# Performance work log

Hardware: AMD Instinct MI355X
Metric: run time of the kernel (lower is better)

The kernel has to match this reference:

```python
import jax, jax.numpy as jnp
import numpy as np


def setup_inputs() -> dict:
    key = jax.random.key(0)
    kx, kb, ky = jax.random.split(key, 3)
    N, K, D = 100000, 256, 3
    x = jax.random.normal(kx, (N, D), dtype=jnp.float32)
    # beta in (0, 1) for atanh; cap below 1 to keep atanh finite
    beta = jax.random.uniform(kb, (N,), dtype=jnp.float32, minval=0.01, maxval=0.95)
    # y in {-1, 0..K-1}; -1 = background. Guarantee both classes present.
    y = jax.random.randint(ky, (N,), -1, K)
    y = y.at[0].set(-1).at[1].set(0)
    return {"x": x, "beta": beta, "y": y, "K": K, "S_b": 1.0, "q_min": 0.5}


def reference(x, beta, y, K, S_b, q_min):
    N = y.shape[0]
    n_i = (y == -1)  # background mask (N,)
    # One-hot membership M_ik (N, K); jax.nn.one_hot gives all-zeros for y == -1
    M = jax.nn.one_hot(y, K, dtype=x.dtype)

    # ---- background loss ----
    beta_ak = jnp.max(beta[:, None] * M, axis=0)               # (K,) segment max
    N_b = jnp.sum(n_i).astype(x.dtype)
    L_beta = jnp.sum(1.0 - beta_ak) / K \
        + (S_b / N_b) * jnp.sum(jnp.where(n_i, beta, 0.0))

    # ---- potential loss ----
    q_i = jnp.square(jnp.arctanh(beta)) + q_min               # (N,) charge
    qM = q_i[:, None] * M                                      # (N, K)
    q_ak = jnp.max(qM, axis=0)                                 # (K,) max charge per cluster
    idx_ak = jnp.argmax(qM, axis=0)                            # (K,) condensation point index
    x_a = x[idx_ak]                                            # (K, D) cluster rep coords
    # pairwise squared distances hit->cluster rep: (N, K)
    x_diff = jnp.sum(jnp.square(x[:, None, :] - x_a[None, :, :]), axis=2)
    x_inv = jnp.maximum(1.0 - x_diff, 0.0)                     # repulsive potential
    # attractive for members, repulsive for non-members, weighted by q_ak and q_i
    per_hit = jnp.sum((M * x_diff + (1.0 - M) * x_inv) * q_ak[None, :], axis=1)
    L_v = jnp.sum(per_hit * q_i) / N

    return L_beta + L_v
```

## Files before the change

### kernel.cpp

```cpp
#include <hip/hip_runtime.h>
#include <math.h>

#define K_MAX 256
#define P1 64
#define NT 256

struct Ws {
    unsigned long long part_packed[P1 * K_MAX];
    unsigned int       part_beta[P1 * K_MAX];
    float              part_bg[P1];
    float              part_nb[P1];
    float4             cvec[K_MAX];
    float              qv[K_MAX];
    float              bak[K_MAX];
    float              bg_total;
    float              nb_total;
};

__device__ __forceinline__ float wave_sum(float v) {
    #pragma unroll
    for (int o = 32; o > 0; o >>= 1) v += __shfl_down(v, o, 64);
    return v;
}

__global__ void __launch_bounds__(NT) k_scan(const float* __restrict__ beta,
        const int* __restrict__ y, const float* __restrict__ qminp,
        Ws* __restrict__ w, int N) {
    __shared__ unsigned long long s_u64[K_MAX];
    __shared__ unsigned int s_u32[K_MAX];
    __shared__ float s_w[8];
    int t = threadIdx.x;
    int b = blockIdx.x;
    s_u64[t] = 0ULL;
    s_u32[t] = 0u;
    __syncthreads();
    float qmin = qminp[0];
    float bg = 0.f, nbc = 0.f;
    for (int i = b * NT + t; i < N; i += P1 * NT) {
        float be = beta[i];
        int yi = y[i];
        if (yi < 0) { bg += be; nbc += 1.f; }
        else {
            atomicMax(&s_u32[yi], __float_as_uint(be));
            float a = atanhf(be);
            float q = fmaf(a, a, qmin);
            unsigned long long p = ((unsigned long long)__float_as_uint(q) << 32)
                                 | (unsigned long long)(~(unsigned int)i);
            atomicMax(&s_u64[yi], p);
        }
    }
    __syncthreads();
    w->part_packed[b * K_MAX + t] = s_u64[t];
    w->part_beta[b * K_MAX + t]  = s_u32[t];
    int lane = t & 63, wid = t >> 6;
    float r1 = wave_sum(bg);
    float r2 = wave_sum(nbc);
    if (lane == 0) { s_w[wid] = r1; s_w[4 + wid] = r2; }
    __syncthreads();
    if (t == 0) w->part_bg[b] = s_w[0] + s_w[1] + s_w[2] + s_w[3];
    if (t == 1) w->part_nb[b] = s_w[4] + s_w[5] + s_w[6] + s_w[7];
}

__global__ void __launch_bounds__(64) k_reduce(const float* __restrict__ x,
        Ws* __restrict__ w, float* __restrict__ out) {
    int b = blockIdx.x, t = threadIdx.x;
    if (b < K_MAX) {
        unsigned long long m = w->part_packed[t * K_MAX + b];
        unsigned int bb = w->part_beta[t * K_MAX + b];
        #pragma unroll
        for (int o = 32; o > 0; o >>= 1) {
            unsigned long long v = __shfl_down(m, o, 64);  if (v > m)  m = v;
            unsigned int       u = __shfl_down(bb, o, 64); if (u > bb) bb = u;
        }
        if (t == 0) {
            float q; unsigned int idx;
            if (m == 0ULL) { q = 0.f; idx = 0u; }
            else { q = __uint_as_float((unsigned int)(m >> 32)); idx = ~(unsigned int)m; }
            float ax = x[idx * 3], ay = x[idx * 3 + 1], az = x[idx * 3 + 2];
            w->cvec[b] = make_float4(2.f * q * ax, 2.f * q * ay, 2.f * q * az,
                                     q * (1.f - (ax * ax + ay * ay + az * az)));
            w->qv[b]  = q;
            w->bak[b] = 1.f - __uint_as_float(bb);
        }
    } else {
        const float* src = (b == K_MAX) ? w->part_bg : w->part_nb;
        float s = wave_sum(src[t]);
        if (t == 0) {
            if (b == K_MAX) { w->bg_total = s; out[0] = 0.f; }
            else            { w->nb_total = s; }
        }
    }
}

__global__ void __launch_bounds__(NT) k_main(const float* __restrict__ x,
        const float* __restrict__ beta, const int* __restrict__ y,
        const int* __restrict__ Kp, const float* __restrict__ Sbp,
        const float* __restrict__ qminp, const Ws* __restrict__ w,
        float* __restrict__ out, int N) {
    __shared__ float4 s_c[K_MAX];
    __shared__ float s_q[K_MAX];
    __shared__ float s_w[8];
    int t = threadIdx.x;
    s_c[t] = w->cvec[t];
    s_q[t] = w->qv[t];
    __syncthreads();
    int i = blockIdx.x * NT + t;
    float contrib = 0.f;
    if (i < N) {
        float x0 = x[i * 3], x1 = x[i * 3 + 1], x2 = x[i * 3 + 2];
        float be = beta[i];
        int yi = y[i];
        float a = atanhf(be);
        float qi = fmaf(a, a, qminp[0]);
        float negh = -(x0 * x0 + x1 * x1 + x2 * x2);
        float acc = 0.f;
        #pragma unroll 8
        for (int k = 0; k < K_MAX; ++k) {
            float4 c = s_c[k];
            float t0 = fmaf(s_q[k], negh, c.w);
            float uq = fmaf(c.x, x0, fmaf(c.y, x1, fmaf(c.z, x2, t0)));
            acc += fmaxf(uq, 0.f);
        }
        if (yi >= 0) {
            float4 c = s_c[yi];
            float qk = s_q[yi];
            float t0 = fmaf(qk, negh, c.w);
            float uq = fmaf(c.x, x0, fmaf(c.y, x1, fmaf(c.z, x2, t0)));
            acc += (qk - uq) - fmaxf(uq, 0.f);
        }
        contrib = acc * qi;
    }
    int lane = t & 63, wid = t >> 6;
    float r = wave_sum(contrib);
    if (lane == 0) s_w[wid] = r;
    __syncthreads();
    if (t == 0) atomicAdd(out, (s_w[0] + s_w[1] + s_w[2] + s_w[3]) * (1.f / (float)N));
    if (blockIdx.x == 0) {
        int K = Kp[0];
        float v = wave_sum((t < K) ? w->bak[t] : 0.f);
        if (lane == 0) s_w[4 + wid] = v;
        __syncthreads();
        if (t == 0) {
            float sb = s_w[4] + s_w[5] + s_w[6] + s_w[7];
            atomicAdd(out, sb / (float)K + Sbp[0] / w->nb_total * w->bg_total);
        }
    }
}

extern "C" void kernel_launch(void* const* d_in, const int* in_sizes, int n_in,
                              void* d_out, int out_size, void* d_ws, size_t ws_size,
                              hipStream_t stream) {
    const float* x     = (const float*)d_in[0];
    const float* beta  = (const float*)d_in[1];
    const int*   y     = (const int*)d_in[2];
    const int*   Kp    = (const int*)d_in[3];
    const float* Sbp   = (const float*)d_in[4];
    const float* qminp = (const float*)d_in[5];
    float* out = (float*)d_out;
    int N = in_sizes[1];
    Ws* w = (Ws*)d_ws;
    int nb = (N + NT - 1) / NT;

    k_scan<<<P1, NT, 0, stream>>>(beta, y, qminp, w, N);
    k_reduce<<<K_MAX + 2, 64, 0, stream>>>(x, w, out);
    k_main<<<nb, NT, 0, stream>>>(x, beta, y, Kp, Sbp, qminp, w, out, N);
}
```

Baseline: 83.53 us.

## Fuse scan, reduce and main kernels into one cooperative kernel with grid syncs

Replaces the three kernel launches with a single cooperative kernel of 256 persistent blocks that uses grid-wide syncs between the segment-max scan, the per-cluster reduction and the main potential pass. The scan now uses 256 blocks instead of 64, and the main pass loops over hits with a grid stride instead of launching one block per 256 hits. The aim is to remove launch gaps and inter-kernel overhead, at the cost of grid-sync latency and a fixed grid that may underuse the GPU for the heavy O(N*K) main loop. The background-beta term is now accumulated with per-cluster atomics.

```diff
diff --git a/kernel.cpp b/kernel.cpp
--- a/kernel.cpp
+++ b/kernel.cpp
@@ -1,20 +1,20 @@
 #include <hip/hip_runtime.h>
+#include <hip/hip_cooperative_groups.h>
 #include <math.h>
 
+namespace cg = cooperative_groups;
+
 #define K_MAX 256
-#define P1 64
+#define NB 256
 #define NT 256
 
 struct Ws {
-    unsigned long long part_packed[P1 * K_MAX];
-    unsigned int       part_beta[P1 * K_MAX];
-    float              part_bg[P1];
-    float              part_nb[P1];
+    unsigned long long part_packed[NB * K_MAX];
+    unsigned int       part_beta[NB * K_MAX];
+    float              part_bg[NB];
+    float              part_nb[NB];
     float4             cvec[K_MAX];
     float              qv[K_MAX];
-    float              bak[K_MAX];
-    float              bg_total;
-    float              nb_total;
 };
 
 __device__ __forceinline__ float wave_sum(float v) {
@@ -23,20 +23,26 @@
     return v;
 }
 
-__global__ void __launch_bounds__(NT) k_scan(const float* __restrict__ beta,
-        const int* __restrict__ y, const float* __restrict__ qminp,
-        Ws* __restrict__ w, int N) {
+__global__ void __launch_bounds__(NT) k_fused(
+        const float* __restrict__ x, const float* __restrict__ beta,
+        const int* __restrict__ y, const int* __restrict__ Kp,
+        const float* __restrict__ Sbp, const float* __restrict__ qminp,
+        Ws* __restrict__ w, float* __restrict__ out, int N) {
     __shared__ unsigned long long s_u64[K_MAX];
     __shared__ unsigned int s_u32[K_MAX];
+    __shared__ float4 s_c[K_MAX];
+    __shared__ float s_q[K_MAX];
     __shared__ float s_w[8];
-    int t = threadIdx.x;
-    int b = blockIdx.x;
+    const int t = threadIdx.x;
+    const int b = blockIdx.x;
+    const int lane = t & 63, wid = t >> 6;
+
     s_u64[t] = 0ULL;
     s_u32[t] = 0u;
     __syncthreads();
-    float qmin = qminp[0];
+    const float qmin = qminp[0];
     float bg = 0.f, nbc = 0.f;
-    for (int i = b * NT + t; i < N; i += P1 * NT) {
+    for (int i = b * NT + t; i < N; i += NB * NT) {
         float be = beta[i];
         int yi = y[i];
         if (yi < 0) { bg += be; nbc += 1.f; }
@@ -52,19 +58,18 @@
     __syncthreads();
     w->part_packed[b * K_MAX + t] = s_u64[t];
     w->part_beta[b * K_MAX + t]  = s_u32[t];
-    int lane = t & 63, wid = t >> 6;
-    float r1 = wave_sum(bg);
-    float r2 = wave_sum(nbc);
-    if (lane == 0) { s_w[wid] = r1; s_w[4 + wid] = r2; }
+    {
+        float r1 = wave_sum(bg), r2 = wave_sum(nbc);
+        if (lane == 0) { s_w[wid] = r1; s_w[4 + wid] = r2; }
+    }
     __syncthreads();
     if (t == 0) w->part_bg[b] = s_w[0] + s_w[1] + s_w[2] + s_w[3];
     if (t == 1) w->part_nb[b] = s_w[4] + s_w[5] + s_w[6] + s_w[7];
-}
+    if (b == 0 && t == 0) out[0] = 0.f;
 
-__global__ void __launch_bounds__(64) k_reduce(const float* __restrict__ x,
-        Ws* __restrict__ w, float* __restrict__ out) {
-    int b = blockIdx.x, t = threadIdx.x;
-    if (b < K_MAX) {
+    cg::this_grid().sync();
+
+    {
         unsigned long long m = w->part_packed[t * K_MAX + b];
         unsigned int bb = w->part_beta[t * K_MAX + b];
         #pragma unroll
@@ -72,46 +77,49 @@
             unsigned long long v = __shfl_down(m, o, 64);  if (v > m)  m = v;
             unsigned int       u = __shfl_down(bb, o, 64); if (u > bb) bb = u;
         }
+        if (lane == 0) { s_u64[wid] = m; s_u32[wid] = bb; }
+        __syncthreads();
         if (t == 0) {
+            m = s_u64[0]; bb = s_u32[0];
+            #pragma unroll
+            for (int q2 = 1; q2 < NT / 64; ++q2) {
+                if (s_u64[q2] > m)  m = s_u64[q2];
+                if (s_u32[q2] > bb) bb = s_u32[q2];
+            }
             float q; unsigned int idx;
             if (m == 0ULL) { q = 0.f; idx = 0u; }
             else { q = __uint_as_float((unsigned int)(m >> 32)); idx = ~(unsigned int)m; }
             float ax = x[idx * 3], ay = x[idx * 3 + 1], az = x[idx * 3 + 2];
             w->cvec[b] = make_float4(2.f * q * ax, 2.f * q * ay, 2.f * q * az,
                                      q * (1.f - (ax * ax + ay * ay + az * az)));
-            w->qv[b]  = q;
-            w->bak[b] = 1.f - __uint_as_float(bb);
+            w->qv[b] = q;
+            atomicAdd(out, (1.f - __uint_as_float(bb)) / (float)Kp[0]);
         }
-    } else {
-        const float* src = (b == K_MAX) ? w->part_bg : w->part_nb;
-        float s = wave_sum(src[t]);
-        if (t == 0) {
-            if (b == K_MAX) { w->bg_total = s; out[0] = 0.f; }
-            else            { w->nb_total = s; }
+        if (b == 0) {
+            float r1 = wave_sum(w->part_bg[t]);
+            float r2 = wave_sum(w->part_nb[t]);
+            if (lane == 0) { s_w[wid] = r1; s_w[4 + wid] = r2; }
+            __syncthreads();
+            if (t == 0) {
+                float bgt = s_w[0] + s_w[1] + s_w[2] + s_w[3];
+                float nbt = s_w[4] + s_w[5] + s_w[6] + s_w[7];
+                atomicAdd(out, Sbp[0] / nbt * bgt);
+            }
         }
     }
-}
 
-__global__ void __launch_bounds__(NT) k_main(const float* __restrict__ x,
-        const float* __restrict__ beta, const int* __restrict__ y,
-        const int* __restrict__ Kp, const float* __restrict__ Sbp,
-        const float* __restrict__ qminp, const Ws* __restrict__ w,
-        float* __restrict__ out, int N) {
-    __shared__ float4 s_c[K_MAX];
-    __shared__ float s_q[K_MAX];
-    __shared__ float s_w[8];
-    int t = threadIdx.x;
+    cg::this_grid().sync();
+
     s_c[t] = w->cvec[t];
     s_q[t] = w->qv[t];
     __syncthreads();
-    int i = blockIdx.x * NT + t;
-    float contrib = 0.f;
-    if (i < N) {
+    float acc_t = 0.f;
+    for (int i = b * NT + t; i < N; i += NB * NT) {
         float x0 = x[i * 3], x1 = x[i * 3 + 1], x2 = x[i * 3 + 2];
         float be = beta[i];
         int yi = y[i];
         float a = atanhf(be);
-        float qi = fmaf(a, a, qminp[0]);
+        float qi = fmaf(a, a, qmin);
         float negh = -(x0 * x0 + x1 * x1 + x2 * x2);
         float acc = 0.f;
         #pragma unroll 8
@@ -128,23 +136,13 @@
             float uq = fmaf(c.x, x0, fmaf(c.y, x1, fmaf(c.z, x2, t0)));
             acc += (qk - uq) - fmaxf(uq, 0.f);
         }
-        contrib = acc * qi;
+        acc_t += acc * qi;
     }
-    int lane = t & 63, wid = t >> 6;
-    float r = wave_sum(contrib);
+    float r = wave_sum(acc_t);
+    __syncthreads();
     if (lane == 0) s_w[wid] = r;
     __syncthreads();
     if (t == 0) atomicAdd(out, (s_w[0] + s_w[1] + s_w[2] + s_w[3]) * (1.f / (float)N));
-    if (blockIdx.x == 0) {
-        int K = Kp[0];
-        float v = wave_sum((t < K) ? w->bak[t] : 0.f);
-        if (lane == 0) s_w[4 + wid] = v;
-        __syncthreads();
-        if (t == 0) {
-            float sb = s_w[4] + s_w[5] + s_w[6] + s_w[7];
-            atomicAdd(out, sb / (float)K + Sbp[0] / w->nb_total * w->bg_total);
-        }
-    }
 }
 
 extern "C" void kernel_launch(void* const* d_in, const int* in_sizes, int n_in,
@@ -159,9 +157,8 @@
     float* out = (float*)d_out;
     int N = in_sizes[1];
     Ws* w = (Ws*)d_ws;
-    int nb = (N + NT - 1) / NT;
 
-    k_scan<<<P1, NT, 0, stream>>>(beta, y, qminp, w, N);
-    k_reduce<<<K_MAX + 2, 64, 0, stream>>>(x, w, out);
-    k_main<<<nb, NT, 0, stream>>>(x, beta, y, Kp, Sbp, qminp, w, out, N);
+    void* args[] = {(void*)&x, (void*)&beta, (void*)&y, (void*)&Kp,
+                    (void*)&Sbp, (void*)&qminp, (void*)&w, (void*)&out, (void*)&N};
+    hipLaunchCooperativeKernel((void*)k_fused, dim3(NB), dim3(NT), args, 0, stream);
 }
```

Result: slower. 143.6 us (+71.9%).
